# Optimization experiments

Measured on AMD Instinct MI355X. Metric: run time of the kernel, lower is better.

Reference implementation:

```python
import jax, jax.numpy as jnp
import numpy as np

B, S, D, H = 4, 2048, 1024, 16
HD = D // H  # head_dim = 64


def setup_inputs() -> dict:
    key = jax.random.key(0)
    ks = jax.random.split(key, 6)
    scale = 1.0 / np.sqrt(D)
    x = jax.random.normal(ks[0], (B, S, D), dtype=jnp.float32)
    mask = jax.random.bernoulli(ks[1], 0.9, (B, S, S))  # bool, True = keep
    wq = jax.random.normal(ks[2], (D, D), dtype=jnp.float32) * scale
    wk = jax.random.normal(ks[3], (D, D), dtype=jnp.float32) * scale
    wv = jax.random.normal(ks[4], (D, D), dtype=jnp.float32) * scale
    wo = jax.random.normal(ks[5], (D, D), dtype=jnp.float32) * scale
    return {"x": x, "mask": mask, "wq": wq, "wk": wk, "wv": wv, "wo": wo}


def reference(x, mask, wq, wk, wv, wo):
    bsz, seqlen, dim = x.shape
    # nn.Linear applies x @ W.T; weights here stored as [out, in]
    xq = (x @ wq.T).reshape(bsz, seqlen, H, HD)
    xk = (x @ wk.T).reshape(bsz, seqlen, H, HD)
    xv = (x @ wv.T).reshape(bsz, seqlen, H, HD)
    # scores: [B, H, S, S]
    scores = jnp.einsum("bqhd,bkhd->bhqk", xq, xk) / np.sqrt(HD).astype(np.float32)
    # additive mask: ~mask * -1e9, broadcast over heads
    neg = jnp.where(mask[:, None, :, :], 0.0, -1e9).astype(scores.dtype)
    scores = scores + neg
    scores = jax.nn.softmax(scores.astype(jnp.float32), axis=-1).astype(xq.dtype)
    # multiplicative re-mask after softmax (as in the original)
    scores = scores * mask[:, None, :, :].astype(scores.dtype)
    out = jnp.einsum("bhqk,bkhd->bqhd", scores, xv).reshape(bsz, seqlen, dim)
    return out @ wo.T
```

## Files before the change

kernel.cpp:

```cpp
#include <hip/hip_runtime.h>
#include <hip/hip_bf16.h>

#define S_LEN 2048
#define DIM   1024
#define NHEAD 16
#define HDIM  64
#define QSCALE 0.18033688f

typedef __attribute__((ext_vector_type(8))) short bfrag;
typedef __attribute__((ext_vector_type(4))) float f32x4;

#define MFMA(a,b,c) __builtin_amdgcn_mfma_f32_16x16x32_bf16((a),(b),(c),0,0,0)

__device__ __forceinline__ unsigned short f2bf(float x) {
  __hip_bfloat16 h = __float2bfloat16(x);
  return *reinterpret_cast<unsigned short*>(&h);
}

__device__ __forceinline__ unsigned int pk2bf(float a, float b) {
  float2 f2; f2.x = a; f2.y = b;
  __hip_bfloat162 b2 = __float22bfloat162_rn(f2);
  return *reinterpret_cast<unsigned int*>(&b2);
}

__device__ __forceinline__ void gll16(const unsigned short* g, unsigned short* l) {
  __builtin_amdgcn_global_load_lds(
      (const __attribute__((address_space(1))) unsigned int*)g,
      (__attribute__((address_space(3))) unsigned int*)l, 16, 0, 0);
}

__global__ void probe(const unsigned int* __restrict__ x,
                      const unsigned int* __restrict__ mask,
                      int* __restrict__ flags) {
  const int lane = threadIdx.x;
  int insane = 0;
  for (int i = lane; i < 512; i += 64) {
    unsigned int w = x[i];
    unsigned int e = (w >> 7) & 0xFFu;
    bool sane = (e >= 90u && e <= 160u) || ((w & 0x7FFFu) == 0u);
    insane += sane ? 0 : 1;
  }
  bool all01 = true, allu8 = true, allf32 = true, allbf = true;
  for (int i = lane; i < 1024; i += 64) {
    unsigned int w = mask[i];
    all01  &= (w <= 1u);
    allu8  &= ((w & 0xFEFEFEFEu) == 0u);
    allf32 &= (w == 0u || w == 0x3F800000u);
    unsigned int lo = w & 0xFFFFu, hi = w >> 16;
    allbf  &= (lo == 0u || lo == 0x3F80u) && (hi == 0u || hi == 0x3F80u);
  }
#pragma unroll
  for (int off = 1; off < 64; off <<= 1) insane += __shfl_xor(insane, off, 64);
  const unsigned long long full = ~0ull;
  const bool g01  = __ballot(all01)  == full;
  const bool gu8  = __ballot(allu8)  == full;
  const bool gf32 = __ballot(allf32) == full;
  const bool gbf  = __ballot(allbf)  == full;
  if (lane == 0) {
    flags[0] = (insane > 128) ? 1 : 0;
    flags[1] = g01 ? 1 : (gu8 ? 0 : (gf32 ? 2 : (gbf ? 3 : 0)));
  }
}

__device__ __forceinline__ bool mask_at(const void* mk, int mode, size_t idx) {
  switch (mode) {
    case 0:  return ((const unsigned char*)mk)[idx]  != 0;
    case 1:  return ((const int*)mk)[idx]            != 0;
    case 2:  return ((const unsigned int*)mk)[idx]   != 0u;
    default: return ((const unsigned short*)mk)[idx] != 0;
  }
}

__global__ __launch_bounds__(256) void cvt_all(
    const void* __restrict__ x,  const void* __restrict__ wq,
    const void* __restrict__ wk, const void* __restrict__ wv,
    const void* __restrict__ wo,
    unsigned short* __restrict__ xb,  unsigned short* __restrict__ wqb,
    unsigned short* __restrict__ wkb, unsigned short* __restrict__ wvb,
    unsigned short* __restrict__ wob, const int* __restrict__ flags) {
  const int bx = blockIdx.x;
  const void* src; unsigned short* dst; int i;
  if (bx < 4096) { src = x; dst = xb; i = bx * 256 + threadIdx.x; }
  else {
    const int r = (bx - 4096) >> 9, off = (bx - 4096) & 511;
    src = r == 0 ? wq : r == 1 ? wk : r == 2 ? wv : wo;
    dst = r == 0 ? wqb : r == 1 ? wkb : r == 2 ? wvb : wob;
    i = off * 256 + threadIdx.x;
  }
  if (flags[0]) {
    const float* p = (const float*)src + (size_t)i * 8;
    float4 a = *reinterpret_cast<const float4*>(p);
    float4 b = *reinterpret_cast<const float4*>(p + 4);
    unsigned int d0 = pk2bf(a.x, a.y), d1 = pk2bf(a.z, a.w);
    unsigned int d2 = pk2bf(b.x, b.y), d3 = pk2bf(b.z, b.w);
    uint4 o; o.x = d0; o.y = d1; o.z = d2; o.w = d3;
    *reinterpret_cast<uint4*>(dst + (size_t)i * 8) = o;
  } else {
    *reinterpret_cast<bfrag*>(dst + (size_t)i * 8) =
        reinterpret_cast<const bfrag*>(src)[i];
  }
}

__global__ __launch_bounds__(256) void bitmask(const void* __restrict__ mk,
                                               const int* __restrict__ flags,
                                               unsigned long long* __restrict__ mb) {
  size_t gid = (size_t)blockIdx.x * 256 + threadIdx.x;
  bool v = mask_at(mk, flags[1], gid);
  unsigned long long w = __ballot(v);
  if ((threadIdx.x & 63) == 0) mb[gid >> 6] = w;
}

__global__ __launch_bounds__(256) void gemm128(const unsigned short* __restrict__ A,
                                               const unsigned short* __restrict__ Bt,
                                               void* __restrict__ C,
                                               const int* __restrict__ flags,
                                               int aHsplit, int cMode) {
  __shared__ unsigned short As[128 * 32];
  __shared__ unsigned short Bs[128 * 32];
  const int t = threadIdx.x, lane = t & 63, wave = t >> 6;
  const int r16 = lane & 15, quad = lane >> 4;
  const int n0 = blockIdx.x * 128, m0 = blockIdx.y * 128;
  const int wm = (wave >> 1) * 64, wn = (wave & 1) * 64;
  const int arow = t >> 2, aseg = (t & 3) * 8;

  f32x4 acc[4][4];
#pragma unroll
  for (int i = 0; i < 4; ++i)
#pragma unroll
    for (int j = 0; j < 4; ++j) acc[i][j] = (f32x4){0.f, 0.f, 0.f, 0.f};

  for (int k0 = 0; k0 < 1024; k0 += 32) {
    __syncthreads();
#pragma unroll
    for (int rr = 0; rr < 2; ++rr) {
      const int m = m0 + rr * 64 + arow;
      const int k = k0 + aseg;
      const unsigned short* ga;
      if (aHsplit) ga = A + ((size_t)(((m >> 11) << 4) + (k >> 6)) * 2048 + (m & 2047)) * 64 + (k & 63);
      else         ga = A + (size_t)m * 1024 + k;
      gll16(ga, As + rr * 2048 + wave * 512);
      const unsigned short* gb = Bt + (size_t)(n0 + rr * 64 + arow) * 1024 + k0 + aseg;
      gll16(gb, Bs + rr * 2048 + wave * 512);
    }
    __syncthreads();

    bfrag af[4], bf[4];
#pragma unroll
    for (int i = 0; i < 4; ++i)
      af[i] = *reinterpret_cast<const bfrag*>(&As[(wm + i * 16 + r16) * 32 + quad * 8]);
#pragma unroll
    for (int j = 0; j < 4; ++j)
      bf[j] = *reinterpret_cast<const bfrag*>(&Bs[(wn + j * 16 + r16) * 32 + quad * 8]);
#pragma unroll
    for (int i = 0; i < 4; ++i)
#pragma unroll
      for (int j = 0; j < 4; ++j)
        acc[i][j] = MFMA(af[i], bf[j], acc[i][j]);
  }

  const int oF = (cMode == 2) ? flags[0] : 0;
#pragma unroll
  for (int i = 0; i < 4; ++i)
#pragma unroll
    for (int j = 0; j < 4; ++j)
#pragma unroll
      for (int r = 0; r < 4; ++r) {
        const int m = m0 + wm + i * 16 + quad * 4 + r;
        const int n = n0 + wn + j * 16 + r16;
        const float v = acc[i][j][r];
        if (cMode == 3) {
          const int region = n >> 10, nn = n & 1023;
          const float vv = (region == 0) ? v * QSCALE : v;
          const size_t idx = (size_t)region * 8388608 +
              ((size_t)((m >> 11) * NHEAD + (nn >> 6)) * 2048 + (m & 2047)) * 64 + (nn & 63);
          ((unsigned short*)C)[idx] = f2bf(vv);
        } else if (cMode == 1) {
          const size_t idx = ((size_t)((m >> 11) * NHEAD + (n >> 6)) * 2048 + (m & 2047)) * 64 + (n & 63);
          ((unsigned short*)C)[idx] = f2bf(v);
        } else {
          const size_t idx = (size_t)m * 1024 + n;
          if (oF) ((float*)C)[idx] = v;
          else    ((unsigned short*)C)[idx] = f2bf(v);
        }
      }
}

__global__ __launch_bounds__(256) void transposeV(const unsigned short* __restrict__ xvH,
                                                  unsigned short* __restrict__ xvT) {
  __shared__ unsigned short Ts[64 * 80];
  const int t = threadIdx.x;
  const int s0 = blockIdx.x * 64, bh = blockIdx.y;
  const int sr = t >> 3, seg = (t & 7) * 8;
#pragma unroll
  for (int rr = 0; rr < 2; ++rr) {
    const int s = rr * 32 + sr;
    bfrag v = *reinterpret_cast<const bfrag*>(xvH + ((size_t)bh * 2048 + s0 + s) * 64 + seg);
#pragma unroll
    for (int j = 0; j < 8; ++j) Ts[(seg + j) * 80 + s] = (unsigned short)v[j];
  }
  __syncthreads();
#pragma unroll
  for (int rr = 0; rr < 2; ++rr) {
    const int d = rr * 32 + sr;
    bfrag o = *reinterpret_cast<const bfrag*>(&Ts[d * 80 + seg]);
    *reinterpret_cast<bfrag*>(xvT + ((size_t)bh * 64 + d) * 2048 + s0 + seg) = o;
  }
}

__global__ __launch_bounds__(256) void fattn(const unsigned short* __restrict__ qH,
                                             const unsigned short* __restrict__ kH,
                                             const unsigned short* __restrict__ vT,
                                             const unsigned long long* __restrict__ mb,
                                             unsigned short* __restrict__ oH) {
  __shared__ unsigned short Ks[2][64 * 64];
  __shared__ unsigned short Vs[2][64 * 64];
  __shared__ unsigned short Ps[4][16 * 72];
  const int t = threadIdx.x, lane = t & 63, wave = t >> 6;
  const int r16 = lane & 15, quad = lane >> 4;
  const int bid = blockIdx.x;
  const int bh = bid & 63, qidx = bid >> 6;
  const int b = bh >> 4;
  const int qw = qidx * 128 + wave * 32;
  const size_t hbase = (size_t)bh * S_LEN;

  bfrag aq[2][2];
#pragma unroll
  for (int qt = 0; qt < 2; ++qt)
#pragma unroll
    for (int hh = 0; hh < 2; ++hh)
      aq[qt][hh] = *reinterpret_cast<const bfrag*>(
          qH + (hbase + qw + qt * 16 + r16) * 64 + hh * 32 + quad * 8);

  f32x4 o[2][4];
#pragma unroll
  for (int qt = 0; qt < 2; ++qt)
#pragma unroll
    for (int i = 0; i < 4; ++i) o[qt][i] = (f32x4){0.f, 0.f, 0.f, 0.f};
  float lsum[2] = {0.f, 0.f};

  const int srow = lane >> 3;
  const int sg   = (lane & 7) ^ srow;

  auto stage = [&](int buf, int kb) {
#pragma unroll
    for (int rr = 0; rr < 2; ++rr) {
      const int row = rr * 32 + wave * 8 + srow;
      gll16(kH + (hbase + kb + row) * 64 + sg * 8, &Ks[buf][rr * 2048 + wave * 512]);
      gll16(vT + ((size_t)bh * 64 + row) * 2048 + kb + sg * 8, &Vs[buf][rr * 2048 + wave * 512]);
    }
  };

  stage(0, 0);
  int cur = 0;
  const unsigned long long* mrow = mb + ((size_t)b * S_LEN + qw + r16) * 32;

  for (int kb = 0; kb < S_LEN; kb += 64) {
    __syncthreads();
    if (kb + 64 < S_LEN) stage(cur ^ 1, kb + 64);

    unsigned long long w01[2];
    w01[0] = mrow[kb >> 6];
    w01[1] = mrow[16 * 32 + (kb >> 6)];

    bfrag kf[4][2], vf[4][2];
#pragma unroll
    for (int t4 = 0; t4 < 4; ++t4)
#pragma unroll
      for (int hh = 0; hh < 2; ++hh) {
        const int ch = (hh * 4 + quad) ^ (r16 & 7);
        kf[t4][hh] = *reinterpret_cast<const bfrag*>(&Ks[cur][(t4 * 16 + r16) * 64 + ch * 8]);
        vf[t4][hh] = *reinterpret_cast<const bfrag*>(&Vs[cur][(t4 * 16 + r16) * 64 + ch * 8]);
      }

#pragma unroll
    for (int qt = 0; qt < 2; ++qt) {
      f32x4 s[4];
#pragma unroll
      for (int t4 = 0; t4 < 4; ++t4) {
        f32x4 z = (f32x4){0.f, 0.f, 0.f, 0.f};
        z = MFMA(kf[t4][0], aq[qt][0], z);
        z = MFMA(kf[t4][1], aq[qt][1], z);
        s[t4] = z;
      }
      const unsigned long long ws = w01[qt] >> (quad * 4);
      const unsigned int wlo = (unsigned int)ws;
      const unsigned int whi = (unsigned int)(ws >> 32);

      float p[4][4];
#pragma unroll
      for (int t4 = 0; t4 < 4; ++t4) {
        const unsigned int word = (t4 < 2) ? wlo : whi;
        const int bpos = (t4 & 1) * 16;
#pragma unroll
        for (int r = 0; r < 4; ++r) {
          const float e = __builtin_amdgcn_exp2f(s[t4][r]);
          const float pv = (word & (1u << (bpos + r))) ? e : 0.f;
          p[t4][r] = pv;
          lsum[qt] += pv;
        }
      }
#pragma unroll
      for (int t4 = 0; t4 < 4; ++t4)
#pragma unroll
        for (int r = 0; r < 4; r += 2)
          *reinterpret_cast<unsigned int*>(
              &Ps[wave][r16 * 72 + t4 * 16 + quad * 4 + r]) = pk2bf(p[t4][r], p[t4][r + 1]);
      __asm__ volatile("s_waitcnt lgkmcnt(0)" ::: "memory");

      bfrag pa0 = *reinterpret_cast<const bfrag*>(&Ps[wave][r16 * 72 + quad * 8]);
      bfrag pa1 = *reinterpret_cast<const bfrag*>(&Ps[wave][r16 * 72 + 32 + quad * 8]);
#pragma unroll
      for (int t4 = 0; t4 < 4; ++t4) {
        o[qt][t4] = MFMA(pa0, vf[t4][0], o[qt][t4]);
        o[qt][t4] = MFMA(pa1, vf[t4][1], o[qt][t4]);
      }
    }
    cur ^= 1;
  }

#pragma unroll
  for (int qt = 0; qt < 2; ++qt) {
    float l = lsum[qt];
    l += __shfl_xor(l, 16, 64);
    l += __shfl_xor(l, 32, 64);
    float rl[4];
#pragma unroll
    for (int r = 0; r < 4; ++r)
      rl[r] = 1.f / fmaxf(__shfl(l, quad * 4 + r, 64), 1e-30f);
#pragma unroll
    for (int t4 = 0; t4 < 4; ++t4)
#pragma unroll
      for (int r = 0; r < 4; ++r)
        oH[(hbase + qw + qt * 16 + quad * 4 + r) * 64 + t4 * 16 + r16] =
            f2bf(o[qt][t4][r] * rl[r]);
  }
}

template<bool F32>
__device__ __forceinline__ bfrag load8(const void* base, size_t idx) {
  if constexpr (F32) {
    const float* p = (const float*)base + idx;
    float4 u = *reinterpret_cast<const float4*>(p);
    float4 v = *reinterpret_cast<const float4*>(p + 4);
    bfrag r;
    r[0]=(short)f2bf(u.x); r[1]=(short)f2bf(u.y); r[2]=(short)f2bf(u.z); r[3]=(short)f2bf(u.w);
    r[4]=(short)f2bf(v.x); r[5]=(short)f2bf(v.y); r[6]=(short)f2bf(v.z); r[7]=(short)f2bf(v.w);
    return r;
  } else {
    return *reinterpret_cast<const bfrag*>((const unsigned short*)base + idx);
  }
}

template<bool AF32, bool BF32>
__device__ __forceinline__ void gemm_body(const void* __restrict__ A, const void* __restrict__ Bt,
                                          void* __restrict__ C, int N, int K, bool outF32) {
  const int lane = threadIdx.x & 63, wave = threadIdx.x >> 6;
  const int r16 = lane & 15, quad = lane >> 4;
  const int m0 = (blockIdx.y * 4 + wave) * 16, n0 = blockIdx.x * 64;
  f32x4 acc[4];
#pragma unroll
  for (int i = 0; i < 4; ++i) acc[i] = (f32x4){0.f,0.f,0.f,0.f};
  const size_t aoff = (size_t)(m0 + r16) * K + quad * 8;
  const size_t boff = (size_t)(n0 + r16) * K + quad * 8;
  for (int k0 = 0; k0 < K; k0 += 32) {
    bfrag a = load8<AF32>(A, aoff + k0);
#pragma unroll
    for (int tt = 0; tt < 4; ++tt) {
      bfrag bb = load8<BF32>(Bt, boff + (size_t)tt * 16 * K + k0);
      acc[tt] = MFMA(a, bb, acc[tt]);
    }
  }
#pragma unroll
  for (int tt = 0; tt < 4; ++tt)
#pragma unroll
    for (int r = 0; r < 4; ++r) {
      const size_t ci = (size_t)(m0 + quad * 4 + r) * N + n0 + tt * 16 + r16;
      if (outF32) ((float*)C)[ci] = acc[tt][r];
      else        ((unsigned short*)C)[ci] = f2bf(acc[tt][r]);
    }
}

__global__ __launch_bounds__(256) void gemm_bt(const void* A, const void* Bt, void* C,
                                               int N, int K, const int* flags,
                                               int aFollows, int outFollows) {
  const int f = flags[0];
  const bool aF = (aFollows != 0) && (f != 0);
  const bool oF = (outFollows != 0) && (f != 0);
  if (f) { if (aF) gemm_body<true, true>(A, Bt, C, N, K, oF);
           else    gemm_body<false, true>(A, Bt, C, N, K, oF); }
  else     gemm_body<false, false>(A, Bt, C, N, K, oF);
}

__global__ __launch_bounds__(64) void fattn_r2(const unsigned short* __restrict__ xq,
                                               const unsigned short* __restrict__ xk,
                                               const unsigned short* __restrict__ xv,
                                               const void* __restrict__ mk,
                                               const int* __restrict__ flags,
                                               unsigned short* __restrict__ xo) {
  __shared__ unsigned short smemP[16 * 32];
  const int lane = threadIdx.x, r16 = lane & 15, quad = lane >> 4;
  const int q0 = blockIdx.x * 16, h = blockIdx.y, b = blockIdx.z;
  const int mmode = flags[1];
  const size_t base = (size_t)b * S_LEN * DIM + (size_t)h * HDIM;
  const size_t mbase = (size_t)b * S_LEN * S_LEN;
  bfrag aq0 = *reinterpret_cast<const bfrag*>(xq + base + (size_t)(q0 + r16) * DIM + quad * 8);
  bfrag aq1 = *reinterpret_cast<const bfrag*>(xq + base + (size_t)(q0 + r16) * DIM + 32 + quad * 8);
  f32x4 o[4];
#pragma unroll
  for (int i = 0; i < 4; ++i) o[i] = (f32x4){0.f,0.f,0.f,0.f};
  float m_r[4] = {-1e30f,-1e30f,-1e30f,-1e30f}, l_r[4] = {0.f,0.f,0.f,0.f};
  for (int kb = 0; kb < S_LEN; kb += 32) {
    const unsigned short* k0p = xk + base + (size_t)(kb + r16) * DIM + quad * 8;
    const unsigned short* k1p = k0p + (size_t)16 * DIM;
    f32x4 s0 = (f32x4){0.f,0.f,0.f,0.f}, s1 = (f32x4){0.f,0.f,0.f,0.f};
    s0 = MFMA(aq0, *reinterpret_cast<const bfrag*>(k0p), s0);
    s0 = MFMA(aq1, *reinterpret_cast<const bfrag*>(k0p + 32), s0);
    s1 = MFMA(aq0, *reinterpret_cast<const bfrag*>(k1p), s1);
    s1 = MFMA(aq1, *reinterpret_cast<const bfrag*>(k1p + 32), s1);
    float l0[4], l1[4], tmax[4];
#pragma unroll
    for (int r = 0; r < 4; ++r) {
      const size_t mrow = mbase + (size_t)(q0 + quad * 4 + r) * S_LEN + kb;
      l0[r] = mask_at(mk, mmode, mrow + r16) ? s0[r] * 0.125f : -1e30f;
      l1[r] = mask_at(mk, mmode, mrow + 16 + r16) ? s1[r] * 0.125f : -1e30f;
      tmax[r] = fmaxf(l0[r], l1[r]);
    }
#pragma unroll
    for (int off = 1; off < 16; off <<= 1)
#pragma unroll
      for (int r = 0; r < 4; ++r) tmax[r] = fmaxf(tmax[r], __shfl_xor(tmax[r], off, 64));
    float p0[4], p1[4], rsum[4];
#pragma unroll
    for (int r = 0; r < 4; ++r) {
      const float mnew = fmaxf(m_r[r], tmax[r]);
      const float alpha = __expf(m_r[r] - mnew);
      m_r[r] = mnew;
      p0[r] = (l0[r] <= -1e29f) ? 0.f : __expf(l0[r] - mnew);
      p1[r] = (l1[r] <= -1e29f) ? 0.f : __expf(l1[r] - mnew);
      rsum[r] = p0[r] + p1[r];
      l_r[r] *= alpha;
#pragma unroll
      for (int tt = 0; tt < 4; ++tt) o[tt][r] *= alpha;
    }
#pragma unroll
    for (int off = 1; off < 16; off <<= 1)
#pragma unroll
      for (int r = 0; r < 4; ++r) rsum[r] += __shfl_xor(rsum[r], off, 64);
#pragma unroll
    for (int r = 0; r < 4; ++r) l_r[r] += rsum[r];
#pragma unroll
    for (int r = 0; r < 4; ++r) {
      smemP[(quad * 4 + r) * 32 + r16] = f2bf(p0[r]);
      smemP[(quad * 4 + r) * 32 + 16 + r16] = f2bf(p1[r]);
    }
    __syncthreads();
    bfrag apf = *reinterpret_cast<const bfrag*>(&smemP[r16 * 32 + quad * 8]);
    const unsigned short* vbase = xv + base + (size_t)(kb + quad * 8) * DIM + r16;
#pragma unroll
    for (int tt = 0; tt < 4; ++tt) {
      bfrag bv;
#pragma unroll
      for (int j = 0; j < 8; ++j) bv[j] = (short)vbase[(size_t)j * DIM + tt * 16];
      o[tt] = MFMA(apf, bv, o[tt]);
    }
    __syncthreads();
  }
#pragma unroll
  for (int tt = 0; tt < 4; ++tt)
#pragma unroll
    for (int r = 0; r < 4; ++r)
      xo[base + (size_t)(q0 + quad * 4 + r) * DIM + tt * 16 + r16] = f2bf(o[tt][r] / l_r[r]);
}

extern "C" void kernel_launch(void* const* d_in, const int* in_sizes, int n_in,
                              void* d_out, int out_size, void* d_ws, size_t ws_size,
                              hipStream_t stream) {
  const void* x  = d_in[0];
  const void* mk = d_in[1];
  const void* wq = d_in[2];
  const void* wk = d_in[3];
  const void* wv = d_in[4];
  const void* wo = d_in[5];

  const size_t MiB = 1048576;
  const size_t NEED = 4096 + 90 * MiB;

  if (ws_size >= NEED) {
    char* p = (char*)d_ws;
    int* flags = (int*)p;                       p += 4096;
    unsigned short* xb  = (unsigned short*)p;   p += 16 * MiB;
    unsigned short* wqb = (unsigned short*)p;   p += 2 * MiB;
    unsigned short* wkb = (unsigned short*)p;   p += 2 * MiB;
    unsigned short* wvb = (unsigned short*)p;   p += 2 * MiB;
    unsigned short* wob = (unsigned short*)p;   p += 2 * MiB;
    unsigned long long* mb = (unsigned long long*)p; p += 2 * MiB;
    unsigned short* xqH = (unsigned short*)p;   p += 16 * MiB;
    unsigned short* xkH = (unsigned short*)p;   p += 16 * MiB;
    unsigned short* xvH = (unsigned short*)p;   p += 16 * MiB;
    unsigned short* xvT = (unsigned short*)p;   p += 16 * MiB;
    unsigned short* xoH = xvH;

    probe<<<1, 64, 0, stream>>>((const unsigned int*)x, (const unsigned int*)mk, flags);
    cvt_all<<<6144, 256, 0, stream>>>(x, wq, wk, wv, wo, xb, wqb, wkb, wvb, wob, flags);
    bitmask<<<65536, 256, 0, stream>>>(mk, flags, mb);

    gemm128<<<dim3(24, 64), 256, 0, stream>>>(xb, wqb, xqH, flags, 0, 3);
    transposeV<<<dim3(32, 64), 256, 0, stream>>>(xvH, xvT);
    fattn<<<dim3(1024), 256, 0, stream>>>(xqH, xkH, xvT, mb, xoH);
    gemm128<<<dim3(8, 64), 256, 0, stream>>>(xoH, wob, d_out, flags, 1, 2);
  } else {
    int* flags = (int*)d_ws;
    unsigned short* xq = (unsigned short*)((char*)d_ws + 256);
    unsigned short* xk = xq + (size_t)8388608;
    unsigned short* xv = xk + (size_t)8388608;
    unsigned short* xo = xv + (size_t)8388608;
    probe<<<1, 64, 0, stream>>>((const unsigned int*)x, (const unsigned int*)mk, flags);
    dim3 gg(16, 128);
    gemm_bt<<<gg, 256, 0, stream>>>(x, wq, xq, 1024, 1024, flags, 1, 0);
    gemm_bt<<<gg, 256, 0, stream>>>(x, wk, xk, 1024, 1024, flags, 1, 0);
    gemm_bt<<<gg, 256, 0, stream>>>(x, wv, xv, 1024, 1024, flags, 1, 0);
    fattn_r2<<<dim3(128, NHEAD, 4), 64, 0, stream>>>(xq, xk, xv, mk, flags, xo);
    gemm_bt<<<gg, 256, 0, stream>>>(xo, wo, d_out, 1024, 1024, flags, 0, 1);
  }
}
```

Before: 430.3 us.

## Switch attention to 32x32x16 MFMA and keep P in registers

```diff
diff --git a/kernel.cpp b/kernel.cpp
--- a/kernel.cpp
+++ b/kernel.cpp
@@ -9,8 +9,11 @@
 
 typedef __attribute__((ext_vector_type(8))) short bfrag;
 typedef __attribute__((ext_vector_type(4))) float f32x4;
-
-#define MFMA(a,b,c) __builtin_amdgcn_mfma_f32_16x16x32_bf16((a),(b),(c),0,0,0)
+typedef __attribute__((ext_vector_type(16))) float f32x16;
+typedef __attribute__((ext_vector_type(4))) unsigned int u32x4;
+
+#define MFMA(a,b,c)   __builtin_amdgcn_mfma_f32_16x16x32_bf16((a),(b),(c),0,0,0)
+#define MFMA32(a,b,c) __builtin_amdgcn_mfma_f32_32x32x16_bf16((a),(b),(c),0,0,0)
 
 __device__ __forceinline__ unsigned short f2bf(float x) {
   __hip_bfloat16 h = __float2bfloat16(x);
@@ -107,7 +110,12 @@
   size_t gid = (size_t)blockIdx.x * 256 + threadIdx.x;
   bool v = mask_at(mk, flags[1], gid);
   unsigned long long w = __ballot(v);
-  if ((threadIdx.x & 63) == 0) mb[gid >> 6] = w;
+  if ((threadIdx.x & 63) == 0) {
+    const size_t bb = gid >> 22;
+    const size_t q  = (gid >> 11) & 2047;
+    const size_t wd = (gid >> 6) & 31;
+    mb[(bb * 32 + wd) * 2048 + q] = w;
+  }
 }
 
 __global__ __launch_bounds__(256) void gemm128(const unsigned short* __restrict__ A,
@@ -210,33 +218,29 @@
 __global__ __launch_bounds__(256) void fattn(const unsigned short* __restrict__ qH,
                                              const unsigned short* __restrict__ kH,
                                              const unsigned short* __restrict__ vT,
-                                             const unsigned long long* __restrict__ mb,
+                                             const unsigned long long* __restrict__ mbT,
                                              unsigned short* __restrict__ oH) {
   __shared__ unsigned short Ks[2][64 * 64];
   __shared__ unsigned short Vs[2][64 * 64];
-  __shared__ unsigned short Ps[4][16 * 72];
   const int t = threadIdx.x, lane = t & 63, wave = t >> 6;
-  const int r16 = lane & 15, quad = lane >> 4;
+  const int l31 = lane & 31, hi = lane >> 5;
   const int bid = blockIdx.x;
   const int bh = bid & 63, qidx = bid >> 6;
   const int b = bh >> 4;
   const int qw = qidx * 128 + wave * 32;
   const size_t hbase = (size_t)bh * S_LEN;
-
-  bfrag aq[2][2];
-#pragma unroll
-  for (int qt = 0; qt < 2; ++qt)
-#pragma unroll
-    for (int hh = 0; hh < 2; ++hh)
-      aq[qt][hh] = *reinterpret_cast<const bfrag*>(
-          qH + (hbase + qw + qt * 16 + r16) * 64 + hh * 32 + quad * 8);
-
-  f32x4 o[2][4];
-#pragma unroll
-  for (int qt = 0; qt < 2; ++qt)
-#pragma unroll
-    for (int i = 0; i < 4; ++i) o[qt][i] = (f32x4){0.f, 0.f, 0.f, 0.f};
-  float lsum[2] = {0.f, 0.f};
+  const int kgr = l31 & 7;
+
+  bfrag qf[4];
+#pragma unroll
+  for (int s = 0; s < 4; ++s)
+    qf[s] = *reinterpret_cast<const bfrag*>(
+        qH + (hbase + qw + l31) * 64 + s * 16 + hi * 8);
+
+  f32x16 o0, o1;
+#pragma unroll
+  for (int r = 0; r < 16; ++r) { o0[r] = 0.f; o1[r] = 0.f; }
+  float lsum = 0.f;
 
   const int srow = lane >> 3;
   const int sg   = (lane & 7) ^ srow;
@@ -252,87 +256,76 @@
 
   stage(0, 0);
   int cur = 0;
-  const unsigned long long* mrow = mb + ((size_t)b * S_LEN + qw + r16) * 32;
+  const unsigned long long* mcol = mbT + (size_t)b * 32 * S_LEN + (qw + l31);
 
   for (int kb = 0; kb < S_LEN; kb += 64) {
     __syncthreads();
     if (kb + 64 < S_LEN) stage(cur ^ 1, kb + 64);
 
-    unsigned long long w01[2];
-    w01[0] = mrow[kb >> 6];
-    w01[1] = mrow[16 * 32 + (kb >> 6)];
-
-    bfrag kf[4][2], vf[4][2];
-#pragma unroll
-    for (int t4 = 0; t4 < 4; ++t4)
-#pragma unroll
-      for (int hh = 0; hh < 2; ++hh) {
-        const int ch = (hh * 4 + quad) ^ (r16 & 7);
-        kf[t4][hh] = *reinterpret_cast<const bfrag*>(&Ks[cur][(t4 * 16 + r16) * 64 + ch * 8]);
-        vf[t4][hh] = *reinterpret_cast<const bfrag*>(&Vs[cur][(t4 * 16 + r16) * 64 + ch * 8]);
+    const unsigned long long w = mcol[(size_t)(kb >> 6) * S_LEN];
+    const unsigned int wlo = (unsigned int)(w >> (4 * hi));
+    const unsigned int whi = (unsigned int)(w >> (32 + 4 * hi));
+
+#pragma unroll
+    for (int c = 0; c < 2; ++c) {
+      f32x16 z;
+#pragma unroll
+      for (int r = 0; r < 16; ++r) z[r] = 0.f;
+#pragma unroll
+      for (int s = 0; s < 4; ++s) {
+        const int gr = (2 * s + hi) ^ kgr;
+        bfrag kf = *reinterpret_cast<const bfrag*>(
+            &Ks[cur][(c * 32 + l31) * 64 + gr * 8]);
+        z = MFMA32(kf, qf[s], z);
       }
-
-#pragma unroll
-    for (int qt = 0; qt < 2; ++qt) {
-      f32x4 s[4];
-#pragma unroll
-      for (int t4 = 0; t4 < 4; ++t4) {
-        f32x4 z = (f32x4){0.f, 0.f, 0.f, 0.f};
-        z = MFMA(kf[t4][0], aq[qt][0], z);
-        z = MFMA(kf[t4][1], aq[qt][1], z);
-        s[t4] = z;
+      const unsigned int wm = c ? whi : wlo;
+#pragma unroll
+      for (int r = 0; r < 16; ++r) {
+        const int bitp = (r & 3) + 8 * (r >> 2);
+        float e = __builtin_amdgcn_exp2f(z[r]);
+        e = (wm & (1u << bitp)) ? e : 0.f;
+        z[r] = e;
+        lsum += e;
       }
-      const unsigned long long ws = w01[qt] >> (quad * 4);
-      const unsigned int wlo = (unsigned int)ws;
-      const unsigned int whi = (unsigned int)(ws >> 32);
-
-      float p[4][4];
-#pragma unroll
-      for (int t4 = 0; t4 < 4; ++t4) {
-        const unsigned int word = (t4 < 2) ? wlo : whi;
-        const int bpos = (t4 & 1) * 16;
-#pragma unroll
-        for (int r = 0; r < 4; ++r) {
-          const float e = __builtin_amdgcn_exp2f(s[t4][r]);
-          const float pv = (word & (1u << (bpos + r))) ? e : 0.f;
-          p[t4][r] = pv;
-          lsum[qt] += pv;
-        }
+      unsigned int pw[8];
+#pragma unroll
+      for (int m = 0; m < 8; ++m)
+        pw[m] = pk2bf(z[2 * m], z[2 * m + 1]);
+
+#pragma unroll
+      for (int s2 = 0; s2 < 2; ++s2) {
+        const int s = 2 * c + s2;
+        const unsigned int b0 = pw[4 * s2 + 0], b1 = pw[4 * s2 + 1];
+        const unsigned int b2 = pw[4 * s2 + 2], b3 = pw[4 * s2 + 3];
+        const unsigned int t0 = __shfl_xor(b0, 32, 64);
+        const unsigned int t1 = __shfl_xor(b1, 32, 64);
+        const unsigned int t2 = __shfl_xor(b2, 32, 64);
+        const unsigned int t3 = __shfl_xor(b3, 32, 64);
+        u32x4 uu;
+        uu.x = hi ? t2 : b0;
+        uu.y = hi ? t3 : b1;
+        uu.z = hi ? b2 : t0;
+        uu.w = hi ? b3 : t1;
+        const bfrag pf = __builtin_bit_cast(bfrag, uu);
+        const int gv = (2 * s + hi) ^ kgr;
+        bfrag v0 = *reinterpret_cast<const bfrag*>(&Vs[cur][l31 * 64 + gv * 8]);
+        bfrag v1 = *reinterpret_cast<const bfrag*>(&Vs[cur][(32 + l31) * 64 + gv * 8]);
+        o0 = MFMA32(pf, v0, o0);
+        o1 = MFMA32(pf, v1, o1);
       }
-#pragma unroll
-      for (int t4 = 0; t4 < 4; ++t4)
-#pragma unroll
-        for (int r = 0; r < 4; r += 2)
-          *reinterpret_cast<unsigned int*>(
-              &Ps[wave][r16 * 72 + t4 * 16 + quad * 4 + r]) = pk2bf(p[t4][r], p[t4][r + 1]);
-      __asm__ volatile("s_waitcnt lgkmcnt(0)" ::: "memory");
-
-      bfrag pa0 = *reinterpret_cast<const bfrag*>(&Ps[wave][r16 * 72 + quad * 8]);
-      bfrag pa1 = *reinterpret_cast<const bfrag*>(&Ps[wave][r16 * 72 + 32 + quad * 8]);
-#pragma unroll
-      for (int t4 = 0; t4 < 4; ++t4) {
-        o[qt][t4] = MFMA(pa0, vf[t4][0], o[qt][t4]);
-        o[qt][t4] = MFMA(pa1, vf[t4][1], o[qt][t4]);
-      }
     }
     cur ^= 1;
   }
 
-#pragma unroll
-  for (int qt = 0; qt < 2; ++qt) {
-    float l = lsum[qt];
-    l += __shfl_xor(l, 16, 64);
-    l += __shfl_xor(l, 32, 64);
-    float rl[4];
-#pragma unroll
-    for (int r = 0; r < 4; ++r)
-      rl[r] = 1.f / fmaxf(__shfl(l, quad * 4 + r, 64), 1e-30f);
-#pragma unroll
-    for (int t4 = 0; t4 < 4; ++t4)
-#pragma unroll
-      for (int r = 0; r < 4; ++r)
-        oH[(hbase + qw + qt * 16 + quad * 4 + r) * 64 + t4 * 16 + r16] =
-            f2bf(o[qt][t4][r] * rl[r]);
+  lsum += __shfl_xor(lsum, 32, 64);
+  const float inv = 1.f / fmaxf(lsum, 1e-30f);
+#pragma unroll
+  for (int r = 0; r < 16; ++r) {
+    const int qr = (r & 3) + 8 * (r >> 2) + 4 * hi;
+    const float sc = __shfl(inv, qr, 64);
+    unsigned short* op = oH + (hbase + qw + qr) * 64 + l31;
+    op[0]  = f2bf(o0[r] * sc);
+    op[32] = f2bf(o1[r] * sc);
   }
 }
 
```

Measured after the change: 437.7 us. No clear change (+1.7%).
